# Performance work log

Hardware: AMD Instinct MI355X
Metric: run time of the kernel (lower is better)

## Reference

```python
import jax, jax.numpy as jnp
import numpy as np

B, L, D, H = 64, 24, 512, 512


def setup_inputs() -> dict:
    key = jax.random.key(0)
    ks = jax.random.split(key, 6)
    inp = jax.random.normal(ks[0], (B, L, D), jnp.float32)
    length = jax.random.randint(ks[1], (B,), L // 2, L + 1)  # valid lengths in [L/2, L]
    # word_linear: word_dim -> 2*hidden_dim (kaiming normal, zero bias)
    word_W = jax.random.normal(ks[2], (2 * H, D), jnp.float32) * (2.0 / D) ** 0.5
    word_b = jnp.zeros((2 * H,), jnp.float32)
    # comp_linear: 2*hidden_dim -> 5*hidden_dim (TreeLSTM gates i, fl, fr, u, o)
    comp_W = jax.random.normal(ks[3], (5 * H, 2 * H), jnp.float32) * (1.0 / H) ** 0.5
    comp_b = jnp.zeros((5 * H,), jnp.float32)
    comp_query = jax.random.normal(ks[4], (H,), jnp.float32) * 0.01
    return dict(inp=inp, length=length, word_W=word_W, word_b=word_b,
                comp_W=comp_W, comp_b=comp_b, comp_query=comp_query)


def _tree_lstm_forward(inp, word_W, word_b, comp_W, comp_b, comp_query, length):
    max_depth = inp.shape[1]
    length_mask = jnp.arange(max_depth)[None, :] < length[:, None]  # (B, L) bool
    # leaf states: word_linear output chunked into (h, c)
    hc = inp @ word_W.T + word_b  # (B, L, 2H)
    h, c = jnp.split(hc, 2, axis=2)
    for i in range(max_depth - 1):  # sequential merge over shrinking length
        hl, cl = h[:, :-1, :], c[:, :-1, :]
        hr, cr = h[:, 1:, :], c[:, 1:, :]
        # BinaryTreeLSTMLayer: fused gate linear on [hl; hr]
        v = jnp.concatenate([hl, hr], axis=2) @ comp_W.T + comp_b  # (B, L-i-1, 5H)
        gi, gfl, gfr, gu, go = jnp.split(v, 5, axis=2)
        new_c = (cl * jax.nn.sigmoid(gfl + 1.0)
                 + cr * jax.nn.sigmoid(gfr + 1.0)
                 + jnp.tanh(gu) * jax.nn.sigmoid(gi))
        new_h = jax.nn.sigmoid(go) * jnp.tanh(new_c)
        if i < max_depth - 2:
            # select_composition: greedy (eval-mode) one-hot over query-dot scores
            scores = jnp.einsum('blh,h->bl', new_h, comp_query)  # (B, L-i-1)
            m = length_mask[:, i + 1:]
            masked = jnp.where(m, scores, -1e9)
            sel = jax.lax.stop_gradient(
                jax.nn.one_hot(jnp.argmax(masked, axis=1), masked.shape[1], dtype=new_h.dtype))
            cum = jnp.cumsum(sel, axis=1)
            left = 1.0 - cum
            right = jnp.concatenate(
                [jnp.zeros((sel.shape[0], 1), sel.dtype), cum[:, :-1]], axis=1)
            new_h = sel[..., None] * new_h + left[..., None] * hl + right[..., None] * hr
            new_c = sel[..., None] * new_c + left[..., None] * cl + right[..., None] * cr
        # update_state: only advance rows whose sequence is still active
        done = length_mask[:, i + 1].astype(new_h.dtype)[:, None, None]
        h = done * new_h + (1.0 - done) * h[:, :-1, :]
        c = done * new_c + (1.0 - done) * c[:, :-1, :]
    return h[:, 0, :]  # (B, H) root hidden state


def reference(inp, length, word_W, word_b, comp_W, comp_b, comp_query):
    return _tree_lstm_forward(inp, word_W, word_b, comp_W, comp_b, comp_query, length)
```

## Files before the change

### kernel.cpp

```cpp
#include <hip/hip_runtime.h>
#include <math.h>

#define BB 64
#define LL 24
#define DD 512
#define GG 2560
#define NSTEP 23
#define NTILES 160

__device__ __forceinline__ float sigm(float x) { return 1.0f / (1.0f + __expf(-x)); }

__device__ __forceinline__ unsigned short f2bf(float x) {
    unsigned u = __float_as_uint(x);
    unsigned r = (u + 0x7fff + ((u >> 16) & 1)) >> 16;
    return (unsigned short)r;
}
__device__ __forceinline__ float bf2f(unsigned short b) {
    return __uint_as_float(((unsigned)b) << 16);
}

using short8 = __attribute__((ext_vector_type(8))) short;
using f32x4 = __attribute__((ext_vector_type(4))) float;

__global__ __launch_bounds__(256) void splitW_k(const float* __restrict__ comp_W,
                                                unsigned short* __restrict__ Wh,
                                                unsigned short* __restrict__ Wl) {
    int t = (blockIdx.x * 256 + threadIdx.x) * 4;
    int n = t >> 9;
    int k = t & 511;
    const float* src = (n < GG) ? (comp_W + (size_t)n * (2 * DD) + k)
                                : (comp_W + (size_t)(n - GG) * (2 * DD) + DD + k);
    float4 v = *(const float4*)src;
    ushort4 h, l;
    h.x = f2bf(v.x); l.x = f2bf(v.x - bf2f(h.x));
    h.y = f2bf(v.y); l.y = f2bf(v.y - bf2f(h.y));
    h.z = f2bf(v.z); l.z = f2bf(v.z - bf2f(h.z));
    h.w = f2bf(v.w); l.w = f2bf(v.w - bf2f(h.w));
    *(ushort4*)(Wh + t) = h;
    *(ushort4*)(Wl + t) = l;
}

__global__ __launch_bounds__(256) void gemm64w(const float* __restrict__ A,
                                               const float* __restrict__ Wt,
                                               const float* __restrict__ bias,
                                               unsigned short* __restrict__ Ah,
                                               unsigned short* __restrict__ Al,
                                               float* __restrict__ O1) {
    __shared__ float As[16][68];
    __shared__ float Bs[16][132];
    const int tid = threadIdx.x;
    const int n0 = blockIdx.x * 128;
    const int m0 = blockIdx.y * 64;
    const int tn = tid & 15;
    const int tm = tid >> 4;

    float acc[4][8];
#pragma unroll
    for (int y = 0; y < 4; ++y)
#pragma unroll
        for (int x = 0; x < 8; ++x) acc[y][x] = 0.f;

    for (int kt = 0; kt < 512; kt += 16) {
        {
            int r = tid >> 2, c4 = tid & 3;
            float4 v = *(const float4*)(A + (size_t)(m0 + r) * DD + kt + c4 * 4);
            As[c4 * 4 + 0][r] = v.x;
            As[c4 * 4 + 1][r] = v.y;
            As[c4 * 4 + 2][r] = v.z;
            As[c4 * 4 + 3][r] = v.w;
        }
#pragma unroll
        for (int ii = 0; ii < 2; ++ii) {
            int idx = tid + ii * 256;
            int r = idx >> 2, c4 = idx & 3;
            float4 v = *(const float4*)(Wt + (size_t)(n0 + r) * DD + kt + c4 * 4);
            Bs[c4 * 4 + 0][r] = v.x;
            Bs[c4 * 4 + 1][r] = v.y;
            Bs[c4 * 4 + 2][r] = v.z;
            Bs[c4 * 4 + 3][r] = v.w;
        }
        __syncthreads();
#pragma unroll
        for (int k = 0; k < 16; ++k) {
            float4 a = *(const float4*)&As[k][tm * 4];
            float4 b0 = *(const float4*)&Bs[k][tn * 4];
            float4 b1 = *(const float4*)&Bs[k][64 + tn * 4];
            float av[4] = {a.x, a.y, a.z, a.w};
            float bv[8] = {b0.x, b0.y, b0.z, b0.w, b1.x, b1.y, b1.z, b1.w};
#pragma unroll
            for (int y = 0; y < 4; ++y)
#pragma unroll
                for (int x = 0; x < 8; ++x) acc[y][x] += av[y] * bv[x];
        }
        __syncthreads();
    }

#pragma unroll
    for (int y = 0; y < 4; ++y) {
        const int m = m0 + tm * 4 + y;
#pragma unroll
        for (int g = 0; g < 2; ++g) {
            int n = n0 + g * 64 + tn * 4;
            float4 v;
            v.x = acc[y][g * 4 + 0] + bias[n + 0];
            v.y = acc[y][g * 4 + 1] + bias[n + 1];
            v.z = acc[y][g * 4 + 2] + bias[n + 2];
            v.w = acc[y][g * 4 + 3] + bias[n + 3];
            if (n < DD) {
                ushort4 hv, lv;
                hv.x = f2bf(v.x); lv.x = f2bf(v.x - bf2f(hv.x));
                hv.y = f2bf(v.y); lv.y = f2bf(v.y - bf2f(hv.y));
                hv.z = f2bf(v.z); lv.z = f2bf(v.z - bf2f(hv.z));
                hv.w = f2bf(v.w); lv.w = f2bf(v.w - bf2f(hv.w));
                *(ushort4*)(Ah + (size_t)m * DD + n) = hv;
                *(ushort4*)(Al + (size_t)m * DD + n) = lv;
            } else {
                *(float4*)(O1 + (size_t)m * DD + (n - DD)) = v;
            }
        }
    }
}

__global__ __launch_bounds__(256) void gemm_big_mfma(
    const unsigned short* __restrict__ Ah, const unsigned short* __restrict__ Al,
    const unsigned short* __restrict__ Wh, const unsigned short* __restrict__ Wl,
    float* __restrict__ O0, float* __restrict__ O1) {
    const int tid = threadIdx.x;
    const int n0 = blockIdx.x * 128;
    const int m0 = blockIdx.y * 128;
    const int w = tid >> 6, lane = tid & 63;
    const int mq = w >> 1, nq = w & 1;
    const int lr = lane & 15, kg = lane >> 4;
    const int kofs = kg * 8;

    const unsigned short* pah[4];
    const unsigned short* pal[4];
    const unsigned short* pbh[4];
    const unsigned short* pbl[4];
#pragma unroll
    for (int t = 0; t < 4; ++t) {
        int mrow = m0 + mq * 64 + t * 16 + lr;
        pah[t] = Ah + (size_t)mrow * DD + kofs;
        pal[t] = Al + (size_t)mrow * DD + kofs;
        int nrow = n0 + nq * 64 + t * 16 + lr;
        pbh[t] = Wh + (size_t)nrow * DD + kofs;
        pbl[t] = Wl + (size_t)nrow * DD + kofs;
    }

    f32x4 acc[4][4];
#pragma unroll
    for (int mt = 0; mt < 4; ++mt)
#pragma unroll
        for (int nt = 0; nt < 4; ++nt) acc[mt][nt] = (f32x4){0.f, 0.f, 0.f, 0.f};

#pragma unroll 2
    for (int ks = 0; ks < 16; ++ks) {
        const int kb = ks * 32;
        short8 ah[4], al[4], bh[4], bl[4];
#pragma unroll
        for (int t = 0; t < 4; ++t) {
            ah[t] = *(const short8*)(pah[t] + kb);
            al[t] = *(const short8*)(pal[t] + kb);
            bh[t] = *(const short8*)(pbh[t] + kb);
            bl[t] = *(const short8*)(pbl[t] + kb);
        }
#pragma unroll
        for (int mt = 0; mt < 4; ++mt)
#pragma unroll
            for (int nt = 0; nt < 4; ++nt) {
                acc[mt][nt] = __builtin_amdgcn_mfma_f32_16x16x32_bf16(al[mt], bh[nt], acc[mt][nt], 0, 0, 0);
                acc[mt][nt] = __builtin_amdgcn_mfma_f32_16x16x32_bf16(ah[mt], bl[nt], acc[mt][nt], 0, 0, 0);
                acc[mt][nt] = __builtin_amdgcn_mfma_f32_16x16x32_bf16(ah[mt], bh[nt], acc[mt][nt], 0, 0, 0);
            }
    }

#pragma unroll
    for (int mt = 0; mt < 4; ++mt) {
        const int mbase = m0 + mq * 64 + mt * 16 + kg * 4;
#pragma unroll
        for (int nt = 0; nt < 4; ++nt) {
            const int n = n0 + nq * 64 + nt * 16 + lr;
#pragma unroll
            for (int r = 0; r < 4; ++r) {
                const int m = mbase + r;
                float* dst = (n < GG) ? (O0 + (size_t)m * GG + n)
                                      : (O1 + (size_t)m * GG + (n - GG));
                *dst = acc[mt][nt][r];
            }
        }
    }
}

__device__ __forceinline__ float half_dot(const float* __restrict__ ar,
                                          const float* __restrict__ br,
                                          const float* __restrict__ cb,
                                          const float* __restrict__ cl,
                                          const float* __restrict__ cr,
                                          const float* __restrict__ q, int lane) {
    float part = 0.f;
#pragma unroll
    for (int d = lane; d < DD; d += 128) {
        float gi = ar[d] + br[d] + cb[d];
        float gfl = ar[DD + d] + br[DD + d] + cb[DD + d];
        float gfr = ar[2 * DD + d] + br[2 * DD + d] + cb[2 * DD + d];
        float gu = ar[3 * DD + d] + br[3 * DD + d] + cb[3 * DD + d];
        float go = ar[4 * DD + d] + br[4 * DD + d] + cb[4 * DD + d];
        float nc = cl[d] * sigm(gfl + 1.f) + cr[d] * sigm(gfr + 1.f) + tanhf(gu) * sigm(gi);
        part += sigm(go) * tanhf(nc) * q[d];
    }
#pragma unroll
    for (int off = 32; off; off >>= 1) part += __shfl_down(part, off);
    return part;
}

__device__ __forceinline__ void gate2n(const float* __restrict__ ar,
                                       const float* __restrict__ br,
                                       const float* __restrict__ cb,
                                       const float* __restrict__ cl,
                                       const float* __restrict__ cr, int d,
                                       float nh[2], float nc[2]) {
    float2 A0 = *(const float2*)(ar + d),          B0 = *(const float2*)(br + d);
    float2 A1 = *(const float2*)(ar + DD + d),     B1 = *(const float2*)(br + DD + d);
    float2 A2 = *(const float2*)(ar + 2 * DD + d), B2 = *(const float2*)(br + 2 * DD + d);
    float2 A3 = *(const float2*)(ar + 3 * DD + d), B3 = *(const float2*)(br + 3 * DD + d);
    float2 A4 = *(const float2*)(ar + 4 * DD + d), B4 = *(const float2*)(br + 4 * DD + d);
    float2 C0 = *(const float2*)(cb + d);
    float2 C1 = *(const float2*)(cb + DD + d);
    float2 C2 = *(const float2*)(cb + 2 * DD + d);
    float2 C3 = *(const float2*)(cb + 3 * DD + d);
    float2 C4 = *(const float2*)(cb + 4 * DD + d);
    float2 CL = *(const float2*)(cl + d);
    float2 CR = *(const float2*)(cr + d);
    float gi0 = A0.x + B0.x + C0.x, gi1 = A0.y + B0.y + C0.y;
    float gfl0 = A1.x + B1.x + C1.x, gfl1 = A1.y + B1.y + C1.y;
    float gfr0 = A2.x + B2.x + C2.x, gfr1 = A2.y + B2.y + C2.y;
    float gu0 = A3.x + B3.x + C3.x, gu1 = A3.y + B3.y + C3.y;
    float go0 = A4.x + B4.x + C4.x, go1 = A4.y + B4.y + C4.y;
    nc[0] = CL.x * sigm(gfl0 + 1.f) + CR.x * sigm(gfr0 + 1.f) + tanhf(gu0) * sigm(gi0);
    nc[1] = CL.y * sigm(gfl1 + 1.f) + CR.y * sigm(gfr1 + 1.f) + tanhf(gu1) * sigm(gi1);
    nh[0] = sigm(go0) * tanhf(nc[0]);
    nh[1] = sigm(go1) * tanhf(nc[1]);
}

__global__ __launch_bounds__(256) void scoreall_k(const float* __restrict__ acache,
                                                  const float* __restrict__ bcache,
                                                  const float* __restrict__ cbuf,
                                                  const float* __restrict__ compb,
                                                  const float* __restrict__ q,
                                                  float* __restrict__ scores_g) {
    __shared__ float red_s[4];
    const int tid = threadIdx.x;
    const int b = blockIdx.y;
    const int p = blockIdx.x * 2 + (tid >> 7);
    const bool valid = p < NSTEP;
    float w = 0.f;
    if (valid) {
        w = half_dot(acache + (size_t)(b * LL + p) * GG,
                     bcache + (size_t)(b * LL + p + 1) * GG, compb,
                     cbuf + (size_t)(b * LL + p) * DD,
                     cbuf + (size_t)(b * LL + p + 1) * DD, q, tid & 127);
    }
    if ((tid & 63) == 0) red_s[tid >> 6] = w;
    __syncthreads();
    if ((tid == 0 || tid == 128) && valid) {
        int base = tid >> 6;
        scores_g[b * NSTEP + p] = red_s[base] + red_s[base + 1];
    }
}

__global__ __launch_bounds__(256) void stepA_k(
    int i, const int* __restrict__ length, float* __restrict__ cbuf,
    const float* __restrict__ acache, const float* __restrict__ bcache,
    float* __restrict__ hout, unsigned short* __restrict__ hh,
    unsigned short* __restrict__ hl, float* __restrict__ scores_g,
    int* __restrict__ seq_g, int* __restrict__ kp_g, int* __restrict__ msel,
    const float* __restrict__ compb, const float* __restrict__ q, float* __restrict__ out) {
    __shared__ float red_s[4];
    __shared__ float sc_l[32];
    __shared__ int seq_l[32];
    __shared__ int k_sh;
    const int tid = threadIdx.x;
    const int b = blockIdx.x;
    const int lane7 = tid & 127;
    const int lenb = length[b];
    const int ncand = NSTEP - i;

    if (i == 0) {
        if (tid < LL) seq_l[tid] = tid;
    } else {
        if (tid < LL - i) seq_l[tid] = seq_g[b * 32 + tid];
    }
    if (tid < ncand) sc_l[tid] = scores_g[b * NSTEP + tid];
    __syncthreads();
    const int kp = (i > 0) ? kp_g[b] : 0;

    if (i > 0 && i < lenb) {
        int p = (tid < 128) ? (kp - 1) : kp;
        bool valid = (p >= 0) && (p < ncand);
        float w = 0.f;
        if (valid) {
            int sl = seq_l[p], sr = seq_l[p + 1];
            const float* ar = acache + (size_t)(b * LL + sl) * GG;
            const float* br = bcache + (size_t)(b * LL + sr) * GG;
            const float* cl = cbuf + (size_t)(b * LL + sl) * DD;
            const float* cr = cbuf + (size_t)(b * LL + sr) * DD;
#pragma unroll
            for (int pass = 0; pass < 2; ++pass) {
                int d = pass * 256 + lane7 * 2;
                float nh[2], nc[2];
                gate2n(ar, br, compb, cl, cr, d, nh, nc);
                float2 Q = *(const float2*)(q + d);
                w += nh[0] * Q.x + nh[1] * Q.y;
            }
#pragma unroll
            for (int off = 32; off; off >>= 1) w += __shfl_down(w, off);
        }
        if ((tid & 63) == 0) red_s[tid >> 6] = w;
        __syncthreads();
        if (tid == 0) {
            if (kp - 1 >= 0) sc_l[kp - 1] = red_s[0] + red_s[1];
            if (kp < ncand) sc_l[kp] = red_s[2] + red_s[3];
        }
        __syncthreads();
    }

    if (i + 1 < lenb) {
        if (tid == 0) {
            const int vmax = lenb - i - 2;
            int k = 0;
            float best = sc_l[0];
            for (int pp = 1; pp <= vmax; ++pp)
                if (sc_l[pp] > best) { best = sc_l[pp]; k = pp; }
            k_sh = k;
        }
        __syncthreads();
        const int k = k_sh;
        const int sl = seq_l[k], sr = seq_l[k + 1];
        const float* ar = acache + (size_t)(b * LL + sl) * GG;
        const float* br = bcache + (size_t)(b * LL + sr) * GG;
        const float* cl = cbuf + (size_t)(b * LL + sl) * DD;
        const float* cr = cbuf + (size_t)(b * LL + sr) * DD;
        {
            const int d = 2 * tid;
            float nh[2], nc[2];
            gate2n(ar, br, compb, cl, cr, d, nh, nc);
            *(float2*)(cbuf + (size_t)(b * LL + sl) * DD + d) = make_float2(nc[0], nc[1]);
            *(float2*)(hout + (size_t)b * DD + d) = make_float2(nh[0], nh[1]);
            ushort2 hv, lv;
            hv.x = f2bf(nh[0]); lv.x = f2bf(nh[0] - bf2f(hv.x));
            hv.y = f2bf(nh[1]); lv.y = f2bf(nh[1] - bf2f(hv.y));
            *(ushort2*)(hh + (size_t)b * DD + d) = hv;
            *(ushort2*)(hl + (size_t)b * DD + d) = lv;
            if (i == NSTEP - 1)
                *(float2*)(out + (size_t)b * DD + d) = make_float2(nh[0], nh[1]);
        }
        float sv = (tid + 1 < ncand) ? sc_l[tid + 1] : 0.f;
        int qv = (tid + 1 < LL - i) ? seq_l[tid + 1] : 0;
        __syncthreads();
        if (tid >= k + 1 && tid <= ncand - 2) sc_l[tid] = sv;
        if (tid >= k + 1 && tid <= LL - i - 2) seq_l[tid] = qv;
        if (tid < ncand - 1) scores_g[b * NSTEP + tid] = sc_l[tid];
        if (tid < LL - i - 1) seq_g[b * 32 + tid] = seq_l[tid];
        if (tid == 0) { kp_g[b] = k; msel[b] = sl; }
    } else if (i == NSTEP - 1) {
        const int d = 2 * tid;
        *(float2*)(out + (size_t)b * DD + d) = *(const float2*)(hout + (size_t)b * DD + d);
    }
}

__global__ __launch_bounds__(256) void stepB_mfma(
    const unsigned short* __restrict__ hh, const unsigned short* __restrict__ hl,
    const int* __restrict__ msel,
    const unsigned short* __restrict__ Wh, const unsigned short* __restrict__ Wl,
    float* __restrict__ acache, float* __restrict__ bcache) {
    __shared__ int msel_s[BB];
    const int tid = threadIdx.x;
    const int bid = blockIdx.x;
    if (tid < BB) msel_s[tid] = msel[tid];
    __syncthreads();

    const int w = tid >> 6, lane = tid & 63;
    const int mt0 = (w >> 1) * 2;
    const int nt = w & 1;
    const int lr = lane & 15;
    const int kg = lane >> 4;
    const int n = bid * 32 + nt * 16 + lr;

    const unsigned short* wh_row = Wh + (size_t)n * DD;
    const unsigned short* wl_row = Wl + (size_t)n * DD;
    const unsigned short* a0h_row = hh + (size_t)(mt0 * 16 + lr) * DD;
    const unsigned short* a0l_row = hl + (size_t)(mt0 * 16 + lr) * DD;
    const unsigned short* a1h_row = a0h_row + 16 * DD;
    const unsigned short* a1l_row = a0l_row + 16 * DD;

    f32x4 acc0 = {0.f, 0.f, 0.f, 0.f};
    f32x4 acc1 = {0.f, 0.f, 0.f, 0.f};

#pragma unroll 4
    for (int ks = 0; ks < 16; ++ks) {
        const int kb = ks * 32 + kg * 8;
        short8 bh = *(const short8*)(wh_row + kb);
        short8 bl = *(const short8*)(wl_row + kb);
        short8 a0h = *(const short8*)(a0h_row + kb);
        short8 a0l = *(const short8*)(a0l_row + kb);
        short8 a1h = *(const short8*)(a1h_row + kb);
        short8 a1l = *(const short8*)(a1l_row + kb);
        acc0 = __builtin_amdgcn_mfma_f32_16x16x32_bf16(a0h, bh, acc0, 0, 0, 0);
        acc1 = __builtin_amdgcn_mfma_f32_16x16x32_bf16(a1h, bh, acc1, 0, 0, 0);
        acc0 = __builtin_amdgcn_mfma_f32_16x16x32_bf16(a0l, bh, acc0, 0, 0, 0);
        acc1 = __builtin_amdgcn_mfma_f32_16x16x32_bf16(a1l, bh, acc1, 0, 0, 0);
        acc0 = __builtin_amdgcn_mfma_f32_16x16x32_bf16(a0h, bl, acc0, 0, 0, 0);
        acc1 = __builtin_amdgcn_mfma_f32_16x16x32_bf16(a1h, bl, acc1, 0, 0, 0);
    }

#pragma unroll
    for (int t = 0; t < 2; ++t) {
        f32x4 acc = t ? acc1 : acc0;
        const int mbase = (mt0 + t) * 16 + kg * 4;
#pragma unroll
        for (int r = 0; r < 4; ++r) {
            int m = mbase + r;
            size_t row = (size_t)(m * LL + msel_s[m]);
            float* dst = (n < GG) ? (acache + row * GG + n)
                                  : (bcache + row * GG + (n - GG));
            *dst = acc[r];
        }
    }
}

extern "C" void kernel_launch(void* const* d_in, const int* in_sizes, int n_in, void* d_out,
                              int out_size, void* d_ws, size_t ws_size, hipStream_t stream) {
    const float* inp = (const float*)d_in[0];
    const int* length = (const int*)d_in[1];
    const float* word_W = (const float*)d_in[2];
    const float* word_b = (const float*)d_in[3];
    const float* comp_W = (const float*)d_in[4];
    const float* comp_b = (const float*)d_in[5];
    const float* comp_q = (const float*)d_in[6];
    float* out = (float*)d_out;

    float* ws = (float*)d_ws;
    size_t off = 0;
    float* cbuf = ws + off;   off += (size_t)BB * LL * DD;
    float* acache = ws + off; off += (size_t)BB * LL * GG;
    float* bcache = ws + off; off += (size_t)BB * LL * GG;
    float* hout = ws + off;   off += (size_t)BB * DD;
    float* scores = ws + off; off += 2048;
    int* seq_g = (int*)(ws + off); off += BB * 32;
    int* kp_g = (int*)(ws + off);  off += 64;
    int* msel = (int*)(ws + off);  off += 64;
    unsigned short* Wh = (unsigned short*)(ws + off); off += (size_t)5120 * DD / 2;
    unsigned short* Wl = (unsigned short*)(ws + off); off += (size_t)5120 * DD / 2;
    unsigned short* hh = (unsigned short*)(ws + off); off += (size_t)BB * DD / 2;
    unsigned short* hl = (unsigned short*)(ws + off); off += (size_t)BB * DD / 2;
    unsigned short* Ah = (unsigned short*)(ws + off); off += (size_t)BB * LL * DD / 2;
    unsigned short* Al = (unsigned short*)(ws + off); off += (size_t)BB * LL * DD / 2;
    (void)ws_size; (void)in_sizes; (void)n_in; (void)out_size;

    splitW_k<<<2560, 256, 0, stream>>>(comp_W, Wh, Wl);

    gemm64w<<<dim3(8, 24), 256, 0, stream>>>(inp, word_W, word_b, Ah, Al, cbuf);

    gemm_big_mfma<<<dim3(40, 12), 256, 0, stream>>>(Ah, Al, Wh, Wl, acache, bcache);

    scoreall_k<<<dim3(12, 64), 256, 0, stream>>>(acache, bcache, cbuf, comp_b, comp_q, scores);

    for (int i = 0; i < NSTEP; ++i) {
        stepA_k<<<BB, 256, 0, stream>>>(i, length, cbuf, acache, bcache, hout, hh, hl,
                                        scores, seq_g, kp_g, msel, comp_b, comp_q, out);
        if (i < NSTEP - 1) {
            stepB_mfma<<<NTILES, 256, 0, stream>>>(hh, hl, msel, Wh, Wl, acache, bcache);
        }
    }
}
```

Baseline: 656.6 us.

## Fuse per-step select and gate GEMM into one cooperative kernel with atomic barrier

Merges the per-step selection kernel (stepA) and the gate-recompute MFMA kernel (stepB) into a single cooperative launch of 224 blocks. The first 64 blocks do selection and publish h with agent-scope atomic stores, then bump striped counters. The remaining 160 blocks prefetch their weight slices and spin on the counters before running the GEMM. This halves the number of launches per step and lets weight loads overlap the selection phase. In exchange it adds spin-wait cost and depends on every block being co-resident.

```diff
diff --git a/kernel.cpp b/kernel.cpp
--- a/kernel.cpp
+++ b/kernel.cpp
@@ -6,7 +6,9 @@
 #define DD 512
 #define GG 2560
 #define NSTEP 23
-#define NTILES 160
+#define NBLKAB 224
+#define NSTRIPES 16
+#define NBSTRIDE 32
 
 __device__ __forceinline__ float sigm(float x) { return 1.0f / (1.0f + __expf(-x)); }
 
@@ -21,6 +23,17 @@
 
 using short8 = __attribute__((ext_vector_type(8))) short;
 using f32x4 = __attribute__((ext_vector_type(4))) float;
+typedef unsigned long long u64;
+
+__device__ __forceinline__ void st4cg(unsigned short* p, unsigned v) {
+    __hip_atomic_store((unsigned*)p, v, __ATOMIC_RELAXED, __HIP_MEMORY_SCOPE_AGENT);
+}
+__device__ __forceinline__ short8 ld8cg(const unsigned short* p) {
+    union { u64 u[2]; short8 v; } t;
+    t.u[0] = __hip_atomic_load((const u64*)p, __ATOMIC_RELAXED, __HIP_MEMORY_SCOPE_AGENT);
+    t.u[1] = __hip_atomic_load((const u64*)p + 1, __ATOMIC_RELAXED, __HIP_MEMORY_SCOPE_AGENT);
+    return t.v;
+}
 
 __global__ __launch_bounds__(256) void splitW_k(const float* __restrict__ comp_W,
                                                 unsigned short* __restrict__ Wh,
@@ -247,11 +260,16 @@
                                                   const float* __restrict__ cbuf,
                                                   const float* __restrict__ compb,
                                                   const float* __restrict__ q,
-                                                  float* __restrict__ scores_g) {
+                                                  float* __restrict__ scores_g,
+                                                  int* __restrict__ barcnt) {
     __shared__ float red_s[4];
     const int tid = threadIdx.x;
     const int b = blockIdx.y;
     const int p = blockIdx.x * 2 + (tid >> 7);
+    if (blockIdx.x == 0 && blockIdx.y == 0) {
+        barcnt[tid] = 0;
+        barcnt[tid + 256] = 0;
+    }
     const bool valid = p < NSTEP;
     float w = 0.f;
     if (valid) {
@@ -268,115 +286,149 @@
     }
 }
 
-__global__ __launch_bounds__(256) void stepA_k(
+__global__ __launch_bounds__(256) void stepAB_k(
     int i, const int* __restrict__ length, float* __restrict__ cbuf,
-    const float* __restrict__ acache, const float* __restrict__ bcache,
+    float* __restrict__ acache, float* __restrict__ bcache,
     float* __restrict__ hout, unsigned short* __restrict__ hh,
     unsigned short* __restrict__ hl, float* __restrict__ scores_g,
     int* __restrict__ seq_g, int* __restrict__ kp_g, int* __restrict__ msel,
-    const float* __restrict__ compb, const float* __restrict__ q, float* __restrict__ out) {
-    __shared__ float red_s[4];
-    __shared__ float sc_l[32];
-    __shared__ int seq_l[32];
-    __shared__ int k_sh;
+    const float* __restrict__ compb, const float* __restrict__ q,
+    float* __restrict__ out,
+    const unsigned short* __restrict__ Wh, const unsigned short* __restrict__ Wl,
+    int* __restrict__ barcnt) {
     const int tid = threadIdx.x;
-    const int b = blockIdx.x;
-    const int lane7 = tid & 127;
-    const int lenb = length[b];
-    const int ncand = NSTEP - i;
-
-    if (i == 0) {
-        if (tid < LL) seq_l[tid] = tid;
-    } else {
-        if (tid < LL - i) seq_l[tid] = seq_g[b * 32 + tid];
-    }
-    if (tid < ncand) sc_l[tid] = scores_g[b * NSTEP + tid];
-    __syncthreads();
-    const int kp = (i > 0) ? kp_g[b] : 0;
-
-    if (i > 0 && i < lenb) {
-        int p = (tid < 128) ? (kp - 1) : kp;
-        bool valid = (p >= 0) && (p < ncand);
-        float w = 0.f;
-        if (valid) {
-            int sl = seq_l[p], sr = seq_l[p + 1];
+    const int bid = blockIdx.x;
+
+    if (bid < BB) {
+        __shared__ float red_s[4];
+        __shared__ float sc_l[32];
+        __shared__ int seq_l[32];
+        __shared__ int k_sh;
+        const int b = bid;
+        const int lane7 = tid & 127;
+        const int lenb = length[b];
+        const int ncand = NSTEP - i;
+
+        if (i == 0) {
+            if (tid < LL) seq_l[tid] = tid;
+        } else {
+            if (tid < LL - i) seq_l[tid] = seq_g[b * 32 + tid];
+        }
+        if (tid < ncand) sc_l[tid] = scores_g[b * NSTEP + tid];
+        __syncthreads();
+        const int kp = (i > 0) ? kp_g[b] : 0;
+
+        if (i > 0 && i < lenb) {
+            int p = (tid < 128) ? (kp - 1) : kp;
+            bool valid = (p >= 0) && (p < ncand);
+            float w = 0.f;
+            if (valid) {
+                int sl = seq_l[p], sr = seq_l[p + 1];
+                const float* ar = acache + (size_t)(b * LL + sl) * GG;
+                const float* br = bcache + (size_t)(b * LL + sr) * GG;
+                const float* cl = cbuf + (size_t)(b * LL + sl) * DD;
+                const float* cr = cbuf + (size_t)(b * LL + sr) * DD;
+#pragma unroll
+                for (int pass = 0; pass < 2; ++pass) {
+                    int d = pass * 256 + lane7 * 2;
+                    float nh[2], nc[2];
+                    gate2n(ar, br, compb, cl, cr, d, nh, nc);
+                    float2 Q = *(const float2*)(q + d);
+                    w += nh[0] * Q.x + nh[1] * Q.y;
+                }
+#pragma unroll
+                for (int off = 32; off; off >>= 1) w += __shfl_down(w, off);
+            }
+            if ((tid & 63) == 0) red_s[tid >> 6] = w;
+            __syncthreads();
+            if (tid == 0) {
+                if (kp - 1 >= 0) sc_l[kp - 1] = red_s[0] + red_s[1];
+                if (kp < ncand) sc_l[kp] = red_s[2] + red_s[3];
+            }
+            __syncthreads();
+        }
+
+        if (i + 1 < lenb) {
+            if (tid == 0) {
+                const int vmax = lenb - i - 2;
+                int k = 0;
+                float best = sc_l[0];
+                for (int pp = 1; pp <= vmax; ++pp)
+                    if (sc_l[pp] > best) { best = sc_l[pp]; k = pp; }
+                k_sh = k;
+            }
+            __syncthreads();
+            const int k = k_sh;
+            const int sl = seq_l[k], sr = seq_l[k + 1];
             const float* ar = acache + (size_t)(b * LL + sl) * GG;
             const float* br = bcache + (size_t)(b * LL + sr) * GG;
             const float* cl = cbuf + (size_t)(b * LL + sl) * DD;
             const float* cr = cbuf + (size_t)(b * LL + sr) * DD;
-#pragma unroll
-            for (int pass = 0; pass < 2; ++pass) {
-                int d = pass * 256 + lane7 * 2;
+            {
+                const int d = 2 * tid;
                 float nh[2], nc[2];
                 gate2n(ar, br, compb, cl, cr, d, nh, nc);
-                float2 Q = *(const float2*)(q + d);
-                w += nh[0] * Q.x + nh[1] * Q.y;
-            }
-#pragma unroll
-            for (int off = 32; off; off >>= 1) w += __shfl_down(w, off);
-        }
-        if ((tid & 63) == 0) red_s[tid >> 6] = w;
+                *(float2*)(cbuf + (size_t)(b * LL + sl) * DD + d) = make_float2(nc[0], nc[1]);
+                *(float2*)(hout + (size_t)b * DD + d) = make_float2(nh[0], nh[1]);
+                ushort2 hv, lv;
+                hv.x = f2bf(nh[0]); lv.x = f2bf(nh[0] - bf2f(hv.x));
+                hv.y = f2bf(nh[1]); lv.y = f2bf(nh[1] - bf2f(hv.y));
+                st4cg(hh + (size_t)b * DD + d, (unsigned)hv.x | ((unsigned)hv.y << 16));
+                st4cg(hl + (size_t)b * DD + d, (unsigned)lv.x | ((unsigned)lv.y << 16));
+                if (i == NSTEP - 1)
+                    *(float2*)(out + (size_t)b * DD + d) = make_float2(nh[0], nh[1]);
+            }
+            float sv = (tid + 1 < ncand) ? sc_l[tid + 1] : 0.f;
+            int qv = (tid + 1 < LL - i) ? seq_l[tid + 1] : 0;
+            __syncthreads();
+            if (tid >= k + 1 && tid <= ncand - 2) sc_l[tid] = sv;
+            if (tid >= k + 1 && tid <= LL - i - 2) seq_l[tid] = qv;
+            if (tid < ncand - 1) scores_g[b * NSTEP + tid] = sc_l[tid];
+            if (tid < LL - i - 1) seq_g[b * 32 + tid] = seq_l[tid];
+            if (tid == 0) {
+                kp_g[b] = k;
+                __hip_atomic_store(msel + b, sl, __ATOMIC_RELAXED, __HIP_MEMORY_SCOPE_AGENT);
+            }
+        } else if (i == NSTEP - 1) {
+            const int d = 2 * tid;
+            *(float2*)(out + (size_t)b * DD + d) = *(const float2*)(hout + (size_t)b * DD + d);
+        }
+
         __syncthreads();
-        if (tid == 0) {
-            if (kp - 1 >= 0) sc_l[kp - 1] = red_s[0] + red_s[1];
-            if (kp < ncand) sc_l[kp] = red_s[2] + red_s[3];
-        }
-        __syncthreads();
-    }
-
-    if (i + 1 < lenb) {
-        if (tid == 0) {
-            const int vmax = lenb - i - 2;
-            int k = 0;
-            float best = sc_l[0];
-            for (int pp = 1; pp <= vmax; ++pp)
-                if (sc_l[pp] > best) { best = sc_l[pp]; k = pp; }
-            k_sh = k;
-        }
-        __syncthreads();
-        const int k = k_sh;
-        const int sl = seq_l[k], sr = seq_l[k + 1];
-        const float* ar = acache + (size_t)(b * LL + sl) * GG;
-        const float* br = bcache + (size_t)(b * LL + sr) * GG;
-        const float* cl = cbuf + (size_t)(b * LL + sl) * DD;
-        const float* cr = cbuf + (size_t)(b * LL + sr) * DD;
-        {
-            const int d = 2 * tid;
-            float nh[2], nc[2];
-            gate2n(ar, br, compb, cl, cr, d, nh, nc);
-            *(float2*)(cbuf + (size_t)(b * LL + sl) * DD + d) = make_float2(nc[0], nc[1]);
-            *(float2*)(hout + (size_t)b * DD + d) = make_float2(nh[0], nh[1]);
-            ushort2 hv, lv;
-            hv.x = f2bf(nh[0]); lv.x = f2bf(nh[0] - bf2f(hv.x));
-            hv.y = f2bf(nh[1]); lv.y = f2bf(nh[1] - bf2f(hv.y));
-            *(ushort2*)(hh + (size_t)b * DD + d) = hv;
-            *(ushort2*)(hl + (size_t)b * DD + d) = lv;
-            if (i == NSTEP - 1)
-                *(float2*)(out + (size_t)b * DD + d) = make_float2(nh[0], nh[1]);
-        }
-        float sv = (tid + 1 < ncand) ? sc_l[tid + 1] : 0.f;
-        int qv = (tid + 1 < LL - i) ? seq_l[tid + 1] : 0;
-        __syncthreads();
-        if (tid >= k + 1 && tid <= ncand - 2) sc_l[tid] = sv;
-        if (tid >= k + 1 && tid <= LL - i - 2) seq_l[tid] = qv;
-        if (tid < ncand - 1) scores_g[b * NSTEP + tid] = sc_l[tid];
-        if (tid < LL - i - 1) seq_g[b * 32 + tid] = seq_l[tid];
-        if (tid == 0) { kp_g[b] = k; msel[b] = sl; }
-    } else if (i == NSTEP - 1) {
-        const int d = 2 * tid;
-        *(float2*)(out + (size_t)b * DD + d) = *(const float2*)(hout + (size_t)b * DD + d);
-    }
-}
-
-__global__ __launch_bounds__(256) void stepB_mfma(
-    const unsigned short* __restrict__ hh, const unsigned short* __restrict__ hl,
-    const int* __restrict__ msel,
-    const unsigned short* __restrict__ Wh, const unsigned short* __restrict__ Wl,
-    float* __restrict__ acache, float* __restrict__ bcache) {
+        if (tid == 0)
+            __hip_atomic_fetch_add(barcnt + (bid & (NSTRIPES - 1)) * NBSTRIDE, 1,
+                                   __ATOMIC_RELEASE, __HIP_MEMORY_SCOPE_AGENT);
+        return;
+    }
+
+    if (i == NSTEP - 1) return;
     __shared__ int msel_s[BB];
-    const int tid = threadIdx.x;
-    const int bid = blockIdx.x;
-    if (tid < BB) msel_s[tid] = msel[tid];
+    const int slice = bid - BB;
+
+    {
+        const float* ph = (const float*)(Wh + (size_t)slice * 32 * DD);
+        const float* pl = (const float*)(Wl + (size_t)slice * 32 * DD);
+        float pf = ph[tid * 32] + pl[tid * 32];
+        asm volatile("" :: "v"(pf));
+    }
+
+    if (tid == 0) {
+        const int target = BB * (i + 1);
+        while (true) {
+            int s = 0;
+#pragma unroll
+            for (int j = 0; j < NSTRIPES; ++j)
+                s += __hip_atomic_load(barcnt + j * NBSTRIDE, __ATOMIC_ACQUIRE,
+                                       __HIP_MEMORY_SCOPE_AGENT);
+            if (s >= target) break;
+            __builtin_amdgcn_s_sleep(2);
+        }
+    }
+    __syncthreads();
+
+    if (tid < BB)
+        msel_s[tid] = __hip_atomic_load(msel + tid, __ATOMIC_RELAXED,
+                                        __HIP_MEMORY_SCOPE_AGENT);
     __syncthreads();
 
     const int w = tid >> 6, lane = tid & 63;
@@ -384,7 +436,7 @@
     const int nt = w & 1;
     const int lr = lane & 15;
     const int kg = lane >> 4;
-    const int n = bid * 32 + nt * 16 + lr;
+    const int n = slice * 32 + nt * 16 + lr;
 
     const unsigned short* wh_row = Wh + (size_t)n * DD;
     const unsigned short* wl_row = Wl + (size_t)n * DD;
@@ -401,10 +453,10 @@
         const int kb = ks * 32 + kg * 8;
         short8 bh = *(const short8*)(wh_row + kb);
         short8 bl = *(const short8*)(wl_row + kb);
-        short8 a0h = *(const short8*)(a0h_row + kb);
-        short8 a0l = *(const short8*)(a0l_row + kb);
-        short8 a1h = *(const short8*)(a1h_row + kb);
-        short8 a1l = *(const short8*)(a1l_row + kb);
+        short8 a0h = ld8cg(a0h_row + kb);
+        short8 a0l = ld8cg(a0l_row + kb);
+        short8 a1h = ld8cg(a1h_row + kb);
+        short8 a1l = ld8cg(a1l_row + kb);
         acc0 = __builtin_amdgcn_mfma_f32_16x16x32_bf16(a0h, bh, acc0, 0, 0, 0);
         acc1 = __builtin_amdgcn_mfma_f32_16x16x32_bf16(a1h, bh, acc1, 0, 0, 0);
         acc0 = __builtin_amdgcn_mfma_f32_16x16x32_bf16(a0l, bh, acc0, 0, 0, 0);
@@ -455,6 +507,7 @@
     unsigned short* hl = (unsigned short*)(ws + off); off += (size_t)BB * DD / 2;
     unsigned short* Ah = (unsigned short*)(ws + off); off += (size_t)BB * LL * DD / 2;
     unsigned short* Al = (unsigned short*)(ws + off); off += (size_t)BB * LL * DD / 2;
+    int* barcnt = (int*)(ws + off); off += 512;
     (void)ws_size; (void)in_sizes; (void)n_in; (void)out_size;
 
     splitW_k<<<2560, 256, 0, stream>>>(comp_W, Wh, Wl);
@@ -463,13 +516,17 @@
 
     gemm_big_mfma<<<dim3(40, 12), 256, 0, stream>>>(Ah, Al, Wh, Wl, acache, bcache);
 
-    scoreall_k<<<dim3(12, 64), 256, 0, stream>>>(acache, bcache, cbuf, comp_b, comp_q, scores);
+    scoreall_k<<<dim3(12, 64), 256, 0, stream>>>(acache, bcache, cbuf, comp_b, comp_q,
+                                                 scores, barcnt);
 
     for (int i = 0; i < NSTEP; ++i) {
-        stepA_k<<<BB, 256, 0, stream>>>(i, length, cbuf, acache, bcache, hout, hh, hl,
-                                        scores, seq_g, kp_g, msel, comp_b, comp_q, out);
-        if (i < NSTEP - 1) {
-            stepB_mfma<<<NTILES, 256, 0, stream>>>(hh, hl, msel, Wh, Wl, acache, bcache);
-        }
-    }
-}
+        int ii = i;
+        void* args[] = {(void*)&ii,     (void*)&length, (void*)&cbuf,   (void*)&acache,
+                        (void*)&bcache, (void*)&hout,   (void*)&hh,     (void*)&hl,
+                        (void*)&scores, (void*)&seq_g,  (void*)&kp_g,   (void*)&msel,
+                        (void*)&comp_b, (void*)&comp_q, (void*)&out,    (void*)&Wh,
+                        (void*)&Wl,     (void*)&barcnt};
+        hipLaunchCooperativeKernel((const void*)stepAB_k, dim3(NBLKAB), dim3(256),
+                                   args, 0, stream);
+    }
+}
```

Result: slower. 1.926 ms (+193.4%).

## Retile big leaf GEMM to 64x128 blocks with XCD-aware swizzle and double-buffered fragments

Applied to the files above, without the earlier changes.

The one-shot leaf-state gate GEMM moves from 128x128 tiles on a 40x12 grid to 64x128 tiles over 960 flat blocks. Block indices are remapped so consecutive blocks land on the same XCD, and each wave now owns a 64x32 sub-tile. Fragment loads are double-buffered, so the next K-slice is fetched while the current one feeds the MFMAs. The goal is more blocks to occupy the CUs and better L2 locality, at the cost of more A reloads per output and extra live registers. This kernel runs once and is a small share of the total time next to the 23 sequential step launches.

```diff
diff --git a/kernel.cpp b/kernel.cpp
--- a/kernel.cpp
+++ b/kernel.cpp
@@ -121,71 +121,97 @@
     }
 }
 
+struct Frag {
+    short8 ah[4], al[4], bh[2], bl[2];
+};
+
+__device__ __forceinline__ void frag_load(Frag& f,
+                                          const unsigned short* const pah[4],
+                                          const unsigned short* const pal[4],
+                                          const unsigned short* const pbh[2],
+                                          const unsigned short* const pbl[2],
+                                          int kb) {
+#pragma unroll
+    for (int t = 0; t < 4; ++t) {
+        f.ah[t] = *(const short8*)(pah[t] + kb);
+        f.al[t] = *(const short8*)(pal[t] + kb);
+    }
+#pragma unroll
+    for (int u = 0; u < 2; ++u) {
+        f.bh[u] = *(const short8*)(pbh[u] + kb);
+        f.bl[u] = *(const short8*)(pbl[u] + kb);
+    }
+}
+
+__device__ __forceinline__ void frag_mma(const Frag& f, f32x4 acc[4][2]) {
+#pragma unroll
+    for (int t = 0; t < 4; ++t)
+#pragma unroll
+        for (int u = 0; u < 2; ++u) {
+            acc[t][u] = __builtin_amdgcn_mfma_f32_16x16x32_bf16(f.al[t], f.bh[u], acc[t][u], 0, 0, 0);
+            acc[t][u] = __builtin_amdgcn_mfma_f32_16x16x32_bf16(f.ah[t], f.bl[u], acc[t][u], 0, 0, 0);
+            acc[t][u] = __builtin_amdgcn_mfma_f32_16x16x32_bf16(f.ah[t], f.bh[u], acc[t][u], 0, 0, 0);
+        }
+}
+
 __global__ __launch_bounds__(256) void gemm_big_mfma(
     const unsigned short* __restrict__ Ah, const unsigned short* __restrict__ Al,
     const unsigned short* __restrict__ Wh, const unsigned short* __restrict__ Wl,
     float* __restrict__ O0, float* __restrict__ O1) {
     const int tid = threadIdx.x;
-    const int n0 = blockIdx.x * 128;
-    const int m0 = blockIdx.y * 128;
+    const int flat = blockIdx.x;
+    const int wg = (flat & 7) * 120 + (flat >> 3);
+    const int m0 = (wg % 24) * 64;
+    const int n0 = (wg / 24) * 128;
     const int w = tid >> 6, lane = tid & 63;
-    const int mq = w >> 1, nq = w & 1;
     const int lr = lane & 15, kg = lane >> 4;
     const int kofs = kg * 8;
 
     const unsigned short* pah[4];
     const unsigned short* pal[4];
-    const unsigned short* pbh[4];
-    const unsigned short* pbl[4];
+    const unsigned short* pbh[2];
+    const unsigned short* pbl[2];
 #pragma unroll
     for (int t = 0; t < 4; ++t) {
-        int mrow = m0 + mq * 64 + t * 16 + lr;
+        int mrow = m0 + t * 16 + lr;
         pah[t] = Ah + (size_t)mrow * DD + kofs;
         pal[t] = Al + (size_t)mrow * DD + kofs;
-        int nrow = n0 + nq * 64 + t * 16 + lr;
-        pbh[t] = Wh + (size_t)nrow * DD + kofs;
-        pbl[t] = Wl + (size_t)nrow * DD + kofs;
-    }
-
-    f32x4 acc[4][4];
-#pragma unroll
-    for (int mt = 0; mt < 4; ++mt)
-#pragma unroll
-        for (int nt = 0; nt < 4; ++nt) acc[mt][nt] = (f32x4){0.f, 0.f, 0.f, 0.f};
-
-#pragma unroll 2
-    for (int ks = 0; ks < 16; ++ks) {
-        const int kb = ks * 32;
-        short8 ah[4], al[4], bh[4], bl[4];
-#pragma unroll
-        for (int t = 0; t < 4; ++t) {
-            ah[t] = *(const short8*)(pah[t] + kb);
-            al[t] = *(const short8*)(pal[t] + kb);
-            bh[t] = *(const short8*)(pbh[t] + kb);
-            bl[t] = *(const short8*)(pbl[t] + kb);
-        }
-#pragma unroll
-        for (int mt = 0; mt < 4; ++mt)
-#pragma unroll
-            for (int nt = 0; nt < 4; ++nt) {
-                acc[mt][nt] = __builtin_amdgcn_mfma_f32_16x16x32_bf16(al[mt], bh[nt], acc[mt][nt], 0, 0, 0);
-                acc[mt][nt] = __builtin_amdgcn_mfma_f32_16x16x32_bf16(ah[mt], bl[nt], acc[mt][nt], 0, 0, 0);
-                acc[mt][nt] = __builtin_amdgcn_mfma_f32_16x16x32_bf16(ah[mt], bh[nt], acc[mt][nt], 0, 0, 0);
-            }
-    }
-
-#pragma unroll
-    for (int mt = 0; mt < 4; ++mt) {
-        const int mbase = m0 + mq * 64 + mt * 16 + kg * 4;
-#pragma unroll
-        for (int nt = 0; nt < 4; ++nt) {
-            const int n = n0 + nq * 64 + nt * 16 + lr;
+    }
+#pragma unroll
+    for (int u = 0; u < 2; ++u) {
+        int nrow = n0 + w * 32 + u * 16 + lr;
+        pbh[u] = Wh + (size_t)nrow * DD + kofs;
+        pbl[u] = Wl + (size_t)nrow * DD + kofs;
+    }
+
+    f32x4 acc[4][2];
+#pragma unroll
+    for (int t = 0; t < 4; ++t)
+#pragma unroll
+        for (int u = 0; u < 2; ++u) acc[t][u] = (f32x4){0.f, 0.f, 0.f, 0.f};
+
+    Frag f0, f1;
+    frag_load(f0, pah, pal, pbh, pbl, 0);
+#pragma unroll
+    for (int ks = 0; ks < 16; ks += 2) {
+        if (ks + 1 < 16) frag_load(f1, pah, pal, pbh, pbl, (ks + 1) * 32);
+        frag_mma(f0, acc);
+        if (ks + 2 < 16) frag_load(f0, pah, pal, pbh, pbl, (ks + 2) * 32);
+        if (ks + 1 < 16) frag_mma(f1, acc);
+    }
+
+#pragma unroll
+    for (int t = 0; t < 4; ++t) {
+        const int mbase = m0 + t * 16 + kg * 4;
+#pragma unroll
+        for (int u = 0; u < 2; ++u) {
+            const int n = n0 + w * 32 + u * 16 + lr;
 #pragma unroll
             for (int r = 0; r < 4; ++r) {
                 const int m = mbase + r;
                 float* dst = (n < GG) ? (O0 + (size_t)m * GG + n)
                                       : (O1 + (size_t)m * GG + (n - GG));
-                *dst = acc[mt][nt][r];
+                *dst = acc[t][u][r];
             }
         }
     }
@@ -461,7 +487,7 @@
 
     gemm64w<<<dim3(8, 24), 256, 0, stream>>>(inp, word_W, word_b, Ah, Al, cbuf);
 
-    gemm_big_mfma<<<dim3(40, 12), 256, 0, stream>>>(Ah, Al, Wh, Wl, acache, bcache);
+    gemm_big_mfma<<<960, 256, 0, stream>>>(Ah, Al, Wh, Wl, acache, bcache);
 
     scoreall_k<<<dim3(12, 64), 256, 0, stream>>>(acache, bcache, cbuf, comp_b, comp_q, scores);
 
```

Result: slower. 687.1 us (+4.6%).

## Stage big GEMM operands through LDS with register prefetch and XCD-aware block mapping

Applied to the files above, without the earlier changes.

The leaf-to-gate GEMM now loads 128x64 tiles of the hi/lo bf16 operands into padded shared memory, prefetching the next k-tile into registers while MFMAs run on the current one. Previously each wave read its fragments straight from global memory with no reuse across waves. The grid is also flattened and remapped so that blocks sharing the same n-columns land on the same XCD, which should improve L2 reuse of W. The cost is about 73 KB of LDS per block, which limits occupancy, plus extra barriers per k-tile.

```diff
diff --git a/kernel.cpp b/kernel.cpp
--- a/kernel.cpp
+++ b/kernel.cpp
@@ -125,27 +125,27 @@
     const unsigned short* __restrict__ Ah, const unsigned short* __restrict__ Al,
     const unsigned short* __restrict__ Wh, const unsigned short* __restrict__ Wl,
     float* __restrict__ O0, float* __restrict__ O1) {
+    __shared__ unsigned short AhS[128][72];
+    __shared__ unsigned short AlS[128][72];
+    __shared__ unsigned short BhS[128][72];
+    __shared__ unsigned short BlS[128][72];
+
     const int tid = threadIdx.x;
-    const int n0 = blockIdx.x * 128;
-    const int m0 = blockIdx.y * 128;
+    const int xcd = blockIdx.x & 7, idx = blockIdx.x >> 3;
+    const int n0 = (xcd * 5 + idx % 5) * 128;
+    const int m0 = (idx / 5) * 128;
+
     const int w = tid >> 6, lane = tid & 63;
     const int mq = w >> 1, nq = w & 1;
     const int lr = lane & 15, kg = lane >> 4;
-    const int kofs = kg * 8;
-
-    const unsigned short* pah[4];
-    const unsigned short* pal[4];
-    const unsigned short* pbh[4];
-    const unsigned short* pbl[4];
-#pragma unroll
-    for (int t = 0; t < 4; ++t) {
-        int mrow = m0 + mq * 64 + t * 16 + lr;
-        pah[t] = Ah + (size_t)mrow * DD + kofs;
-        pal[t] = Al + (size_t)mrow * DD + kofs;
-        int nrow = n0 + nq * 64 + t * 16 + lr;
-        pbh[t] = Wh + (size_t)nrow * DD + kofs;
-        pbl[t] = Wl + (size_t)nrow * DD + kofs;
-    }
+
+    const int srow = tid >> 3;
+    const int sk8 = tid & 7;
+
+    const unsigned short* agh = Ah + (size_t)(m0 + srow) * DD + sk8 * 8;
+    const unsigned short* agl = Al + (size_t)(m0 + srow) * DD + sk8 * 8;
+    const unsigned short* bgh = Wh + (size_t)(n0 + srow) * DD + sk8 * 8;
+    const unsigned short* bgl = Wl + (size_t)(n0 + srow) * DD + sk8 * 8;
 
     f32x4 acc[4][4];
 #pragma unroll
@@ -153,26 +153,65 @@
 #pragma unroll
         for (int nt = 0; nt < 4; ++nt) acc[mt][nt] = (f32x4){0.f, 0.f, 0.f, 0.f};
 
-#pragma unroll 2
-    for (int ks = 0; ks < 16; ++ks) {
-        const int kb = ks * 32;
-        short8 ah[4], al[4], bh[4], bl[4];
-#pragma unroll
-        for (int t = 0; t < 4; ++t) {
-            ah[t] = *(const short8*)(pah[t] + kb);
-            al[t] = *(const short8*)(pal[t] + kb);
-            bh[t] = *(const short8*)(pbh[t] + kb);
-            bl[t] = *(const short8*)(pbl[t] + kb);
-        }
-#pragma unroll
-        for (int mt = 0; mt < 4; ++mt)
-#pragma unroll
-            for (int nt = 0; nt < 4; ++nt) {
-                acc[mt][nt] = __builtin_amdgcn_mfma_f32_16x16x32_bf16(al[mt], bh[nt], acc[mt][nt], 0, 0, 0);
-                acc[mt][nt] = __builtin_amdgcn_mfma_f32_16x16x32_bf16(ah[mt], bl[nt], acc[mt][nt], 0, 0, 0);
-                acc[mt][nt] = __builtin_amdgcn_mfma_f32_16x16x32_bf16(ah[mt], bh[nt], acc[mt][nt], 0, 0, 0);
+    short8 rAh[4], rAl[4], rBh[4], rBl[4];
+
+#define LOADT(kt)                                                            \
+    {                                                                        \
+        _Pragma("unroll")                                                    \
+        for (int it = 0; it < 4; ++it) {                                     \
+            const size_t ro = (size_t)it * 32 * DD + (kt);                   \
+            rAh[it] = *(const short8*)(agh + ro);                            \
+            rAl[it] = *(const short8*)(agl + ro);                            \
+            rBh[it] = *(const short8*)(bgh + ro);                            \
+            rBl[it] = *(const short8*)(bgl + ro);                            \
+        }                                                                    \
+    }
+#define WRITET()                                                             \
+    {                                                                        \
+        _Pragma("unroll")                                                    \
+        for (int it = 0; it < 4; ++it) {                                     \
+            const int row = srow + it * 32;                                  \
+            *(short8*)&AhS[row][sk8 * 8] = rAh[it];                          \
+            *(short8*)&AlS[row][sk8 * 8] = rAl[it];                          \
+            *(short8*)&BhS[row][sk8 * 8] = rBh[it];                          \
+            *(short8*)&BlS[row][sk8 * 8] = rBl[it];                          \
+        }                                                                    \
+    }
+
+    LOADT(0);
+    WRITET();
+    __syncthreads();
+
+    for (int kti = 0; kti < 8; ++kti) {
+        if (kti + 1 < 8) LOADT((kti + 1) * 64);
+#pragma unroll
+        for (int ks2 = 0; ks2 < 2; ++ks2) {
+            const int kb = ks2 * 32 + kg * 8;
+            short8 fah[4], fal[4], fbh[4], fbl[4];
+#pragma unroll
+            for (int t = 0; t < 4; ++t) {
+                fah[t] = *(const short8*)&AhS[mq * 64 + t * 16 + lr][kb];
+                fal[t] = *(const short8*)&AlS[mq * 64 + t * 16 + lr][kb];
+                fbh[t] = *(const short8*)&BhS[nq * 64 + t * 16 + lr][kb];
+                fbl[t] = *(const short8*)&BlS[nq * 64 + t * 16 + lr][kb];
             }
-    }
+#pragma unroll
+            for (int mt = 0; mt < 4; ++mt)
+#pragma unroll
+                for (int nt = 0; nt < 4; ++nt) {
+                    acc[mt][nt] = __builtin_amdgcn_mfma_f32_16x16x32_bf16(fal[mt], fbh[nt], acc[mt][nt], 0, 0, 0);
+                    acc[mt][nt] = __builtin_amdgcn_mfma_f32_16x16x32_bf16(fah[mt], fbl[nt], acc[mt][nt], 0, 0, 0);
+                    acc[mt][nt] = __builtin_amdgcn_mfma_f32_16x16x32_bf16(fah[mt], fbh[nt], acc[mt][nt], 0, 0, 0);
+                }
+        }
+        __syncthreads();
+        if (kti + 1 < 8) {
+            WRITET();
+            __syncthreads();
+        }
+    }
+#undef LOADT
+#undef WRITET
 
 #pragma unroll
     for (int mt = 0; mt < 4; ++mt) {
@@ -461,7 +500,7 @@
 
     gemm64w<<<dim3(8, 24), 256, 0, stream>>>(inp, word_W, word_b, Ah, Al, cbuf);
 
-    gemm_big_mfma<<<dim3(40, 12), 256, 0, stream>>>(Ah, Al, Wh, Wl, acache, bcache);
+    gemm_big_mfma<<<480, 256, 0, stream>>>(Ah, Al, Wh, Wl, acache, bcache);
 
     scoreall_k<<<dim3(12, 64), 256, 0, stream>>>(acache, bcache, cbuf, comp_b, comp_q, scores);
 
```

Measured after the change: 625.2 us. 1.05x faster.
